# Kernel tuning notes

Hardware: AMD Instinct MI355X
Metric: run time of the kernel (lower is better)

## Reference

```python
import jax, jax.numpy as jnp
import numpy as np

LAMB = 5.0
B, N = 1024, 3125  # batch, anchors (5 anchors x 25x25 map)

def setup_inputs() -> dict:
    key = jax.random.key(0)
    k1, k2, k3, k4 = jax.random.split(key, 4)
    return {
        "c_pred": jax.random.normal(k1, (B, N, 2), dtype=jnp.float32),
        "r_pred": jax.random.normal(k2, (B, N, 4), dtype=jnp.float32),
        "r_target": jax.random.normal(k3, (B, N, 4), dtype=jnp.float32),
        # anchor labels in {-1: ignore, 0: negative, 1: positive}
        "label": jax.random.randint(k4, (B, N), -1, 2, dtype=jnp.int32),
    }

def reference(c_pred, r_pred, r_target, label):
    dt = c_pred.dtype
    pos = (label == 1)
    neg = (label == 0)
    pos_cnt = pos.sum(axis=-1).astype(dt)  # [B]
    neg_cnt = neg.sum(axis=-1).astype(dt)

    # --- classification: masked 2-class cross-entropy, pos/neg balanced per batch ---
    logp = jax.nn.log_softmax(c_pred, axis=-1)  # [B, N, 2]
    ce_pos = -logp[..., 1]                      # CE when target class = 1
    ce_neg = -logp[..., 0]                      # CE when target class = 0
    pos_mean = jnp.where(pos_cnt > 0,
                         (ce_pos * pos).sum(axis=-1) / jnp.maximum(pos_cnt, 1.0), 0.0)
    neg_mean = (ce_neg * neg).sum(axis=-1) / jnp.maximum(neg_cnt, 1.0)
    c_loss = ((pos_mean + neg_mean) * 0.5).mean()

    d = r_pred - r_target
    a = jnp.abs(d)
    sl = jnp.where(a < 1.0, 0.5 * d * d, a - 0.5)  # [B, N, 4]
    # per-batch mean over pos_num*4 elements == masked mean of per-anchor coord-mean
    r_per = (sl.mean(axis=-1) * pos).sum(axis=-1) / jnp.maximum(pos_cnt, 1.0)
    r_loss = jnp.where(pos_cnt > 0, r_per, 0.0).mean()

    t_loss = c_loss + LAMB * r_loss
    return (c_loss, r_loss, t_loss)
```

## Files before the change

kernel.cpp:

```cpp
#include <hip/hip_runtime.h>

#define BATCH 1024
#define NANCH 3125
#define LAMB 5.0f

__device__ __forceinline__ float wave_red_f(float v) {
    #pragma unroll
    for (int o = 32; o > 0; o >>= 1) v += __shfl_down(v, o, 64);
    return v;
}
__device__ __forceinline__ int wave_red_i(int v) {
    #pragma unroll
    for (int o = 32; o > 0; o >>= 1) v += __shfl_down(v, o, 64);
    return v;
}

__global__ __launch_bounds__(256) void per_batch_kernel(
    const float* __restrict__ c_pred,
    const float* __restrict__ r_pred,
    const float* __restrict__ r_target,
    const int*   __restrict__ label,
    float2*      __restrict__ per_batch)
{
    const int b   = blockIdx.x;
    const int tid = threadIdx.x;

    const float2* c2 = (const float2*)(c_pred   + (size_t)b * NANCH * 2);
    const float4* rp = (const float4*)(r_pred   + (size_t)b * NANCH * 4);
    const float4* rt = (const float4*)(r_target + (size_t)b * NANCH * 4);
    const int*    lb = label + (size_t)b * NANCH;

    float ce_pos_sum = 0.f, ce_neg_sum = 0.f, sl_sum = 0.f;
    int   pos_cnt = 0, neg_cnt = 0;

    for (int i = tid; i < NANCH; i += 256) {
        const int l = lb[i];
        const float2 c = c2[i];
        const float m   = fmaxf(c.x, c.y);
        const float lse = m + log1pf(__expf(-fabsf(c.x - c.y)));
        if (l == 1) {
            pos_cnt++;
            ce_pos_sum += lse - c.y;
            const float4 p = rp[i];
            const float4 t = rt[i];
            float s = 0.f, d, a;
            d = p.x - t.x; a = fabsf(d); s += (a < 1.f) ? 0.5f * d * d : a - 0.5f;
            d = p.y - t.y; a = fabsf(d); s += (a < 1.f) ? 0.5f * d * d : a - 0.5f;
            d = p.z - t.z; a = fabsf(d); s += (a < 1.f) ? 0.5f * d * d : a - 0.5f;
            d = p.w - t.w; a = fabsf(d); s += (a < 1.f) ? 0.5f * d * d : a - 0.5f;
            sl_sum += s * 0.25f;
        } else if (l == 0) {
            neg_cnt++;
            ce_neg_sum += lse - c.x;
        }
    }

    ce_pos_sum = wave_red_f(ce_pos_sum);
    ce_neg_sum = wave_red_f(ce_neg_sum);
    sl_sum     = wave_red_f(sl_sum);
    pos_cnt    = wave_red_i(pos_cnt);
    neg_cnt    = wave_red_i(neg_cnt);

    __shared__ float s_cp[4], s_cn[4], s_sl[4];
    __shared__ int   s_pc[4], s_nc[4];
    const int wid = tid >> 6, lane = tid & 63;
    if (lane == 0) {
        s_cp[wid] = ce_pos_sum; s_cn[wid] = ce_neg_sum; s_sl[wid] = sl_sum;
        s_pc[wid] = pos_cnt;    s_nc[wid] = neg_cnt;
    }
    __syncthreads();
    if (tid == 0) {
        float cp = 0.f, cn = 0.f, sl = 0.f; int pc = 0, nc = 0;
        #pragma unroll
        for (int w = 0; w < 4; ++w) {
            cp += s_cp[w]; cn += s_cn[w]; sl += s_sl[w];
            pc += s_pc[w]; nc += s_nc[w];
        }
        const float pcf = (float)pc, ncf = (float)nc;
        const float pos_mean = (pc > 0) ? cp / fmaxf(pcf, 1.f) : 0.f;
        const float neg_mean = cn / fmaxf(ncf, 1.f);
        const float c_contrib = (pos_mean + neg_mean) * 0.5f;
        const float r_contrib = (pc > 0) ? sl / fmaxf(pcf, 1.f) : 0.f;
        per_batch[b] = make_float2(c_contrib, r_contrib);
    }
}

__global__ __launch_bounds__(256) void finalize_kernel(
    const float2* __restrict__ per_batch,
    float*        __restrict__ out)
{
    const int tid = threadIdx.x;
    float c = 0.f, r = 0.f;
    #pragma unroll
    for (int i = tid; i < BATCH; i += 256) {
        const float2 v = per_batch[i];
        c += v.x; r += v.y;
    }
    c = wave_red_f(c);
    r = wave_red_f(r);
    __shared__ float s_c[4], s_r[4];
    const int wid = tid >> 6, lane = tid & 63;
    if (lane == 0) { s_c[wid] = c; s_r[wid] = r; }
    __syncthreads();
    if (tid == 0) {
        float cs = 0.f, rs = 0.f;
        #pragma unroll
        for (int w = 0; w < 4; ++w) { cs += s_c[w]; rs += s_r[w]; }
        const float c_loss = cs / (float)BATCH;
        const float r_loss = rs / (float)BATCH;
        out[0] = c_loss;
        out[1] = r_loss;
        out[2] = c_loss + LAMB * r_loss;
    }
}

extern "C" void kernel_launch(void* const* d_in, const int* in_sizes, int n_in,
                              void* d_out, int out_size, void* d_ws, size_t ws_size,
                              hipStream_t stream) {
    const float* c_pred   = (const float*)d_in[0];
    const float* r_pred   = (const float*)d_in[1];
    const float* r_target = (const float*)d_in[2];
    const int*   label    = (const int*)d_in[3];
    float*       out      = (float*)d_out;
    float2*      per_batch = (float2*)d_ws;

    per_batch_kernel<<<BATCH, 256, 0, stream>>>(c_pred, r_pred, r_target, label, per_batch);
    finalize_kernel<<<1, 256, 0, stream>>>(per_batch, out);
}
```

Before: 30.05 us.

## Split each batch across four blocks and make the per-anchor loss branchless

The per-batch kernel now launches BATCH*SPLIT blocks, each reducing a quarter of the anchors into five raw partial sums: CE sums, smooth-L1 sum, and pos/neg counts held as floats. The finalize kernel combines the partials per batch and applies the masked means. The inner loop now loads r_pred/r_target for every anchor and masks with 0/1 multipliers instead of branching, which removes wave divergence. The cost is extra loads and arithmetic for non-positive anchors, a larger partial buffer, and more serial work in the single-block finalize. Float counts stay exact at these sizes.

```diff
diff --git a/kernel.cpp b/kernel.cpp
--- a/kernel.cpp
+++ b/kernel.cpp
@@ -2,27 +2,26 @@
 
 #define BATCH 1024
 #define NANCH 3125
-#define LAMB 5.0f
+#define LAMB  5.0f
+#define SPLIT 4
+#define CHUNK ((NANCH + SPLIT - 1) / SPLIT)
 
 __device__ __forceinline__ float wave_red_f(float v) {
     #pragma unroll
     for (int o = 32; o > 0; o >>= 1) v += __shfl_down(v, o, 64);
     return v;
 }
-__device__ __forceinline__ int wave_red_i(int v) {
-    #pragma unroll
-    for (int o = 32; o > 0; o >>= 1) v += __shfl_down(v, o, 64);
-    return v;
-}
 
-__global__ __launch_bounds__(256) void per_batch_kernel(
+__global__ __launch_bounds__(256) void partial_kernel(
     const float* __restrict__ c_pred,
     const float* __restrict__ r_pred,
     const float* __restrict__ r_target,
     const int*   __restrict__ label,
-    float2*      __restrict__ per_batch)
+    float*       __restrict__ partial)
 {
-    const int b   = blockIdx.x;
+    const int blk = blockIdx.x;
+    const int b   = blk / SPLIT;
+    const int s   = blk % SPLIT;
     const int tid = threadIdx.x;
 
     const float2* c2 = (const float2*)(c_pred   + (size_t)b * NANCH * 2);
@@ -30,77 +29,87 @@
     const float4* rt = (const float4*)(r_target + (size_t)b * NANCH * 4);
     const int*    lb = label + (size_t)b * NANCH;
 
-    float ce_pos_sum = 0.f, ce_neg_sum = 0.f, sl_sum = 0.f;
-    int   pos_cnt = 0, neg_cnt = 0;
+    const int end = min((s + 1) * CHUNK, NANCH);
 
-    for (int i = tid; i < NANCH; i += 256) {
-        const int l = lb[i];
+    float cp = 0.f, cn = 0.f, sl = 0.f, pc = 0.f, nc = 0.f;
+
+    for (int i = s * CHUNK + tid; i < end; i += 256) {
+        const int    l = lb[i];
         const float2 c = c2[i];
+        const float4 p = rp[i];
+        const float4 t = rt[i];
+
+        const float isp = (l == 1) ? 1.f : 0.f;
+        const float isn = (l == 0) ? 1.f : 0.f;
+
         const float m   = fmaxf(c.x, c.y);
         const float lse = m + log1pf(__expf(-fabsf(c.x - c.y)));
-        if (l == 1) {
-            pos_cnt++;
-            ce_pos_sum += lse - c.y;
-            const float4 p = rp[i];
-            const float4 t = rt[i];
-            float s = 0.f, d, a;
-            d = p.x - t.x; a = fabsf(d); s += (a < 1.f) ? 0.5f * d * d : a - 0.5f;
-            d = p.y - t.y; a = fabsf(d); s += (a < 1.f) ? 0.5f * d * d : a - 0.5f;
-            d = p.z - t.z; a = fabsf(d); s += (a < 1.f) ? 0.5f * d * d : a - 0.5f;
-            d = p.w - t.w; a = fabsf(d); s += (a < 1.f) ? 0.5f * d * d : a - 0.5f;
-            sl_sum += s * 0.25f;
-        } else if (l == 0) {
-            neg_cnt++;
-            ce_neg_sum += lse - c.x;
-        }
+
+        pc += isp;
+        nc += isn;
+        cp += isp * (lse - c.y);
+        cn += isn * (lse - c.x);
+
+        float s4 = 0.f, d, a;
+        d = p.x - t.x; a = fabsf(d); s4 += (a < 1.f) ? 0.5f * d * d : a - 0.5f;
+        d = p.y - t.y; a = fabsf(d); s4 += (a < 1.f) ? 0.5f * d * d : a - 0.5f;
+        d = p.z - t.z; a = fabsf(d); s4 += (a < 1.f) ? 0.5f * d * d : a - 0.5f;
+        d = p.w - t.w; a = fabsf(d); s4 += (a < 1.f) ? 0.5f * d * d : a - 0.5f;
+        sl += isp * s4 * 0.25f;
     }
 
-    ce_pos_sum = wave_red_f(ce_pos_sum);
-    ce_neg_sum = wave_red_f(ce_neg_sum);
-    sl_sum     = wave_red_f(sl_sum);
-    pos_cnt    = wave_red_i(pos_cnt);
-    neg_cnt    = wave_red_i(neg_cnt);
+    cp = wave_red_f(cp);
+    cn = wave_red_f(cn);
+    sl = wave_red_f(sl);
+    pc = wave_red_f(pc);
+    nc = wave_red_f(nc);
 
-    __shared__ float s_cp[4], s_cn[4], s_sl[4];
-    __shared__ int   s_pc[4], s_nc[4];
+    __shared__ float sm[5][4];
     const int wid = tid >> 6, lane = tid & 63;
     if (lane == 0) {
-        s_cp[wid] = ce_pos_sum; s_cn[wid] = ce_neg_sum; s_sl[wid] = sl_sum;
-        s_pc[wid] = pos_cnt;    s_nc[wid] = neg_cnt;
+        sm[0][wid] = cp; sm[1][wid] = cn; sm[2][wid] = sl;
+        sm[3][wid] = pc; sm[4][wid] = nc;
     }
     __syncthreads();
     if (tid == 0) {
-        float cp = 0.f, cn = 0.f, sl = 0.f; int pc = 0, nc = 0;
+        float v0 = 0.f, v1 = 0.f, v2 = 0.f, v3 = 0.f, v4 = 0.f;
         #pragma unroll
         for (int w = 0; w < 4; ++w) {
-            cp += s_cp[w]; cn += s_cn[w]; sl += s_sl[w];
-            pc += s_pc[w]; nc += s_nc[w];
+            v0 += sm[0][w]; v1 += sm[1][w]; v2 += sm[2][w];
+            v3 += sm[3][w]; v4 += sm[4][w];
         }
-        const float pcf = (float)pc, ncf = (float)nc;
-        const float pos_mean = (pc > 0) ? cp / fmaxf(pcf, 1.f) : 0.f;
-        const float neg_mean = cn / fmaxf(ncf, 1.f);
-        const float c_contrib = (pos_mean + neg_mean) * 0.5f;
-        const float r_contrib = (pc > 0) ? sl / fmaxf(pcf, 1.f) : 0.f;
-        per_batch[b] = make_float2(c_contrib, r_contrib);
+        float* o = partial + (size_t)blk * 5;
+        o[0] = v0; o[1] = v1; o[2] = v2; o[3] = v3; o[4] = v4;
     }
 }
 
 __global__ __launch_bounds__(256) void finalize_kernel(
-    const float2* __restrict__ per_batch,
-    float*        __restrict__ out)
+    const float* __restrict__ partial,
+    float*       __restrict__ out)
 {
     const int tid = threadIdx.x;
-    float c = 0.f, r = 0.f;
-    #pragma unroll
-    for (int i = tid; i < BATCH; i += 256) {
-        const float2 v = per_batch[i];
-        c += v.x; r += v.y;
+    float csum = 0.f, rsum = 0.f;
+
+    for (int b = tid; b < BATCH; b += 256) {
+        float cp = 0.f, cn = 0.f, sl = 0.f, pc = 0.f, nc = 0.f;
+        #pragma unroll
+        for (int s = 0; s < SPLIT; ++s) {
+            const float* p = partial + ((size_t)b * SPLIT + s) * 5;
+            cp += p[0]; cn += p[1]; sl += p[2]; pc += p[3]; nc += p[4];
+        }
+        const bool haspos = (pc > 0.5f);
+        const float pos_mean = haspos ? cp / fmaxf(pc, 1.f) : 0.f;
+        const float neg_mean = cn / fmaxf(nc, 1.f);
+        csum += (pos_mean + neg_mean) * 0.5f;
+        rsum += haspos ? sl / fmaxf(pc, 1.f) : 0.f;
     }
-    c = wave_red_f(c);
-    r = wave_red_f(r);
+
+    csum = wave_red_f(csum);
+    rsum = wave_red_f(rsum);
+
     __shared__ float s_c[4], s_r[4];
     const int wid = tid >> 6, lane = tid & 63;
-    if (lane == 0) { s_c[wid] = c; s_r[wid] = r; }
+    if (lane == 0) { s_c[wid] = csum; s_r[wid] = rsum; }
     __syncthreads();
     if (tid == 0) {
         float cs = 0.f, rs = 0.f;
@@ -122,8 +131,8 @@
     const float* r_target = (const float*)d_in[2];
     const int*   label    = (const int*)d_in[3];
     float*       out      = (float*)d_out;
-    float2*      per_batch = (float2*)d_ws;
+    float*       partial  = (float*)d_ws;
 
-    per_batch_kernel<<<BATCH, 256, 0, stream>>>(c_pred, r_pred, r_target, label, per_batch);
-    finalize_kernel<<<1, 256, 0, stream>>>(per_batch, out);
+    partial_kernel<<<BATCH * SPLIT, 256, 0, stream>>>(c_pred, r_pred, r_target, label, partial);
+    finalize_kernel<<<1, 256, 0, stream>>>(partial, out);
 }
```

New measurement: 32.37 us. 7.7% more time.
